# Optimization experiments

Measured on AMD Instinct MI355X. Metric: run time of the kernel, lower is better.

The kernel has to match this reference:

```python
import jax, jax.numpy as jnp
import numpy as np
import math

B, D, OUT = 512, 128, 100000
S, M = 32.0, 0.5
COS_M, SIN_M = math.cos(M), math.sin(M)
TH = math.cos(math.pi - M)
MM = math.sin(math.pi - M) * M
M1 = M2 = M3 = M5 = 1.0


def setup_inputs() -> dict:
    key = jax.random.key(0)
    k1, k2, k3, k4, k5, k6 = jax.random.split(key, 6)
    x = jax.random.normal(k1, (B, D), dtype=jnp.float32)
    label = jax.random.randint(k2, (B,), 0, OUT)
    k = jax.random.uniform(k3, (1, 1, 1024, 1024), dtype=jnp.float32)
    x0 = jax.random.uniform(k4, (1, 3, 112, 96), dtype=jnp.float32)
    img = jax.random.uniform(k5, (1, 3, 112, 96), dtype=jnp.float32)
    # xavier_uniform for [OUT, D]
    limit = math.sqrt(6.0 / (OUT + D))
    W = jax.random.uniform(k6, (OUT, D), minval=-limit, maxval=limit, dtype=jnp.float32)
    return {"x": x, "label": label, "k": k, "x0": x0, "img": img, "W": W}


def _arcmargin(x, W, label):
    xn = x / jnp.linalg.norm(x, axis=-1, keepdims=True)
    wn = W / jnp.linalg.norm(W, axis=-1, keepdims=True)
    cosine = xn @ wn.T                                  # [B, OUT]
    sine = jnp.sqrt(jnp.clip(1.0 - cosine * cosine, 0.0))
    phi = cosine * COS_M - sine * SIN_M
    phi = jnp.where(cosine - TH > 0, phi, cosine - MM)   # easy_margin=False
    one_hot = jax.nn.one_hot(label, OUT, dtype=cosine.dtype)
    logits = S * (one_hot * phi + (1.0 - one_hot) * cosine)
    logp = jax.nn.log_softmax(logits, axis=-1)
    return -jnp.mean(jnp.take_along_axis(logp, label[:, None], axis=1))


def _tv_loss(k):
    h, w = k.shape[-2], k.shape[-1]
    count_h = (h - 1) * w
    count_w = h * (w - 1)
    h_tv = jnp.sum((k[:, :, 1:, :] - k[:, :, :-1, :]) ** 2)
    w_tv = jnp.sum((k[:, :, :, 1:] - k[:, :, :, :-1]) ** 2)
    return -1.0 * 2.0 * (h_tv / count_h + w_tv / count_w)  # weight = -1*loss_weight


def _bin_loss(k):
    # sum over pixels of k^2 + (k-1)^2, / (h*w), then mean over batch/channel
    return jnp.mean(k * k + (k - 1.0) ** 2)


def _inv_loss(k):
    k = jax.lax.stop_gradient(k)  # original detaches before numpy FFT
    mag = jnp.abs(jnp.fft.fftn(k, axes=(-2, -1)))
    return jnp.mean(jnp.sum(mag, axis=(-1, -2)))  # L1 norm over (-1,-2), then mean


def reference(x, label, k, x0, img, W):
    loss = (M1 * _arcmargin(x, W, label)
            + M2 * _tv_loss(k)
            + M3 * _bin_loss(k)
            + M5 * _inv_loss(k))
    return loss
```

## Files before the change

kernel.cpp:

```cpp
#include <hip/hip_runtime.h>


typedef short bf16x8 __attribute__((ext_vector_type(8)));
typedef float f32x4 __attribute__((ext_vector_type(4)));
typedef unsigned short u16;
typedef unsigned int u32;

#define BATCH 512
#define DIM 128
#define OUTN 100000
#define OUTPAD 100096
#define NOBLK 782
#define NROW2 1564
#define CHUNKS 16
#define CHSZ2 98
#define SSCALE 32.0f
#define K2C 46.166241308446828f
#define COSM 0.8775825618903728f
#define SINM 0.479425538604203f
#define THC (-0.8775825618903728f)
#define MMC 0.2397127693021015f

#define S1_FFT 1024
#define S1_TV  2048
#define S1_XP  2176
#define S1_NW  14688

#define S2_GEMM0 256
#define S2_NBLK  3392

__device__ inline u16 f2bf(float f) {
  union { float f; u32 u; } v; v.f = f;
  u32 r = v.u + 0x7FFFu + ((v.u >> 16) & 1u);
  return (u16)(r >> 16);
}

__device__ inline float waveRedSum(float v) {
#pragma unroll
  for (int off = 1; off < 64; off <<= 1) v += __shfl_xor(v, off, 64);
  return v;
}

__device__ inline float halfRedSum(float v) {
#pragma unroll
  for (int off = 1; off < 32; off <<= 1) v += __shfl_xor(v, off, 64);
  return v;
}

__global__ __launch_bounds__(256) void stage1_k(const float* __restrict__ x,
                                                const float* __restrict__ W,
                                                const int* __restrict__ label,
                                                const float* __restrict__ kimg,
                                                u32* __restrict__ xh,
                                                float* __restrict__ coslab,
                                                u32* __restrict__ Wh,
                                                float4* __restrict__ tvpart,
                                                float2* __restrict__ fbuf) {
  __shared__ __align__(16) float smem[2064];
  int t = threadIdx.x;
  int bid = blockIdx.x;

  if (bid < S1_FFT) {
    float* re = smem;
    float* im = smem + 1024;
    int r = bid;
#pragma unroll
    for (int i = 0; i < 4; i++) {
      int idx = i * 256 + t;
      re[idx] = kimg[r * 1024 + idx];
      im[idx] = 0.f;
    }
    __syncthreads();
    for (int lh = 9; lh >= 0; lh--) {
      int hlf = 1 << lh;
      float ang = -6.283185307179586f / (float)(hlf * 2);
#pragma unroll
      for (int i = 0; i < 2; i++) {
        int bf = i * 256 + t;
        int pos = bf & (hlf - 1);
        int g = bf >> lh;
        int i0 = (g << (lh + 1)) + pos;
        int i1 = i0 + hlf;
        float ur = re[i0], ui = im[i0], vr = re[i1], vi = im[i1];
        float s, c;
        __sincosf(ang * (float)pos, &s, &c);
        re[i0] = ur + vr; im[i0] = ui + vi;
        float dr = ur - vr, di = ui - vi;
        re[i1] = dr * c - di * s;
        im[i1] = dr * s + di * c;
      }
      __syncthreads();
    }
#pragma unroll
    for (int i = 0; i < 4; i++) {
      int idx = i * 256 + t;
      fbuf[(size_t)r * 1024 + idx] = make_float2(re[idx], im[idx]);
    }
  } else if (bid < S1_TV) {
    int r = bid - S1_FFT;
    int idx = r * 1024 + t * 4;
    float4 v = *(const float4*)&kimg[idx];
    float bs = v.x * v.x + (v.x - 1.f) * (v.x - 1.f)
             + v.y * v.y + (v.y - 1.f) * (v.y - 1.f)
             + v.z * v.z + (v.z - 1.f) * (v.z - 1.f)
             + v.w * v.w + (v.w - 1.f) * (v.w - 1.f);
    float d0 = v.y - v.x, d1 = v.z - v.y, d2 = v.w - v.z;
    float wsm = d0 * d0 + d1 * d1 + d2 * d2;
    if (t < 255) { float e4 = kimg[idx + 4]; float d3 = e4 - v.w; wsm += d3 * d3; }
    float hs = 0.f;
    if (r < 1023) {
      float4 n = *(const float4*)&kimg[idx + 1024];
      float h0 = n.x - v.x, h1 = n.y - v.y, h2 = n.z - v.z, h3 = n.w - v.w;
      hs = h0 * h0 + h1 * h1 + h2 * h2 + h3 * h3;
    }
    hs = waveRedSum(hs); wsm = waveRedSum(wsm); bs = waveRedSum(bs);
    float (*red)[4] = (float(*)[4])smem;
    if ((t & 63) == 0) { int w = t >> 6; red[0][w] = hs; red[1][w] = wsm; red[2][w] = bs; }
    __syncthreads();
    if (t == 0)
      tvpart[r] = make_float4(red[0][0] + red[0][1] + red[0][2] + red[0][3],
                              red[1][0] + red[1][1] + red[1][2] + red[1][3],
                              red[2][0] + red[2][1] + red[2][2] + red[2][3], 0.f);
  } else if (bid < S1_XP) {
    int b = (bid - S1_TV) * 4 + (t >> 6);
    int lane = t & 63;
    size_t xb = (size_t)b * DIM;
    float2 v = *(const float2*)&x[xb + lane * 2];
    int lab = label[b];
    size_t wb = (size_t)lab * DIM;
    float2 w = *(const float2*)&W[wb + lane * 2];
    float ss = waveRedSum(v.x * v.x + v.y * v.y);
    float d  = waveRedSum(v.x * w.x + v.y * w.y);
    float nw = waveRedSum(w.x * w.x + w.y * w.y);
    float inv = rsqrtf(ss);
    xh[b * 64 + lane] = (u32)f2bf(v.x * inv) | ((u32)f2bf(v.y * inv) << 16);
    if (lane == 0) coslab[b] = d * rsqrtf(ss * nw);
  } else {
    int p = (bid - S1_XP) * 4 + (t >> 6);
    int lane = t & 63;
    if (2 * p >= OUTN) {
      *(uint2*)&Wh[(size_t)p * 128 + lane * 2] = make_uint2(0u, 0u);
      return;
    }
    float4 v = *(const float4*)&W[(size_t)p * 256 + lane * 4];
    float ss = halfRedSum(v.x * v.x + v.y * v.y + v.z * v.z + v.w * v.w);
    float inv = rsqrtf(ss);
    u32 lo = (u32)f2bf(v.x * inv) | ((u32)f2bf(v.y * inv) << 16);
    u32 hi = (u32)f2bf(v.z * inv) | ((u32)f2bf(v.w * inv) << 16);
    *(uint2*)&Wh[(size_t)p * 128 + lane * 2] = make_uint2(lo, hi);
  }
}

__global__ __launch_bounds__(256, 4) void stage2_k(const u16* __restrict__ Wh,
                                                   const u16* __restrict__ xh,
                                                   float* __restrict__ gpart,
                                                   const float2* __restrict__ fbuf,
                                                   float* __restrict__ fftpart) {
  __shared__ __align__(16) char smem[32784];
  int t = threadIdx.x;
  int bid = blockIdx.x;

  if (bid >= S2_GEMM0) {
    int wgrp = (bid - S2_GEMM0) & 31, g = (bid - S2_GEMM0) >> 5;
    int o = g * 8 + (wgrp & 7), bt = wgrp >> 3;
    if (o >= NOBLK) return;
    int o0 = o * 128, b0 = bt * 128;
    u16* Ash = (u16*)smem;
    u16* Bsh = (u16*)(smem + 16384);
    int wv = t >> 6, lane = t & 63;
    int wo = (wv & 1) << 6, wbs = (wv >> 1) << 6;
    int m16 = lane & 15, q = lane >> 4;
    f32x4 acc[4][4] = {};

#pragma unroll
    for (int kc = 0; kc < 2; kc++) {
      if (kc) __syncthreads();
#pragma unroll
      for (int i = 0; i < 4; i++) {
        int f = i * 256 + t;
        int rr = f >> 3, gg = f & 7;
        int sw = ((gg ^ (rr & 7)) * 8);
        *(uint4*)&Ash[rr * 64 + sw] =
            *(const uint4*)&Wh[(size_t)(o0 + rr) * DIM + kc * 64 + gg * 8];
        *(uint4*)&Bsh[rr * 64 + sw] =
            *(const uint4*)&xh[(size_t)(b0 + rr) * DIM + kc * 64 + gg * 8];
      }
      __syncthreads();
#pragma unroll
      for (int kk = 0; kk < 2; kk++) {
        bf16x8 af[4], bfr[4];
#pragma unroll
        for (int i = 0; i < 4; i++) {
          int row = wo + i * 16 + m16;
          af[i] = *(const bf16x8*)&Ash[row * 64 + (((kk * 4 + q) ^ (row & 7)) * 8)];
        }
#pragma unroll
        for (int j = 0; j < 4; j++) {
          int row = wbs + j * 16 + m16;
          bfr[j] = *(const bf16x8*)&Bsh[row * 64 + (((kk * 4 + q) ^ (row & 7)) * 8)];
        }
#pragma unroll
        for (int i = 0; i < 4; i++)
#pragma unroll
          for (int j = 0; j < 4; j++)
            acc[i][j] = __builtin_amdgcn_mfma_f32_16x16x32_bf16(af[i], bfr[j], acc[i][j], 0, 0, 0);
      }
    }
#pragma unroll
    for (int j = 0; j < 4; j++) {
      float s = 0.f;
#pragma unroll
      for (int i = 0; i < 4; i++)
#pragma unroll
        for (int r = 0; r < 4; r++)
          s += exp2f(K2C * acc[i][j][r]);
      s += __shfl_xor(s, 16, 64);
      s += __shfl_xor(s, 32, 64);
      if (q == 0)
        gpart[(size_t)(o * 2 + (wv & 1)) * 512 + b0 + wbs + j * 16 + m16] = s;
    }
  } else {
    float2* arr = (float2*)smem;
    float* red = (float*)(smem + 32768);
    int c0 = bid * 4;
#pragma unroll
    for (int i = 0; i < 16; i++) {
      int li = i * 256 + t;
      int rr = li >> 2, c = li & 3;
      arr[rr * 4 + c] = fbuf[(size_t)rr * 1024 + c0 + c];
    }
    __syncthreads();
    for (int lh = 9; lh >= 0; lh--) {
      int hlf = 1 << lh;
      float ang = -6.283185307179586f / (float)(hlf * 2);
#pragma unroll
      for (int i = 0; i < 8; i++) {
        int w = i * 256 + t;
        int c = w & 3, bf = w >> 2;
        int pos = bf & (hlf - 1), g2i = bf >> lh;
        int i0 = ((g2i << (lh + 1)) + pos) * 4 + c;
        int i1 = i0 + hlf * 4;
        float2 u = arr[i0], v = arr[i1];
        float s, cc;
        __sincosf(ang * (float)pos, &s, &cc);
        arr[i0] = make_float2(u.x + v.x, u.y + v.y);
        float dr = u.x - v.x, di = u.y - v.y;
        arr[i1] = make_float2(dr * cc - di * s, dr * s + di * cc);
      }
      __syncthreads();
    }
    float s = 0.f;
#pragma unroll
    for (int i = 0; i < 16; i++) {
      float2 v = arr[i * 256 + t];
      s += sqrtf(v.x * v.x + v.y * v.y);
    }
    s = waveRedSum(s);
    if ((t & 63) == 0) red[t >> 6] = s;
    __syncthreads();
    if (t == 0) fftpart[bid] = red[0] + red[1] + red[2] + red[3];
  }
}

__global__ __launch_bounds__(256) void gemmred_k(const float* __restrict__ gpart,
                                                 float* __restrict__ g2,
                                                 const u32* __restrict__ xh32,
                                                 const u32* __restrict__ Wh32,
                                                 const int* __restrict__ label,
                                                 float* __restrict__ labexp) {
  int t = threadIdx.x;
  int blk = blockIdx.x;
  if (blk < 32) {
    int chunk = blk >> 1, half = blk & 1;
    int b = half * 256 + t;
    int rBeg = chunk * CHSZ2;
    int rEnd = rBeg + CHSZ2; if (rEnd > NROW2) rEnd = NROW2;
    float s = 0.f;
    for (int r = rBeg; r < rEnd; r++) s += gpart[(size_t)r * 512 + b];
    g2[chunk * 512 + b] = s;
  } else {
    int b = (blk - 32) * 256 + t;
    int lab = label[b];
    const u32* xr = &xh32[b * 64];
    const u32* wr = &Wh32[(size_t)lab * 64];
    float d = 0.f;
#pragma unroll 8
    for (int i = 0; i < 64; i++) {
      u32 xa = xr[i], wa = wr[i];
      float xl = __uint_as_float(xa << 16), xhp = __uint_as_float(xa & 0xFFFF0000u);
      float wl = __uint_as_float(wa << 16), whp = __uint_as_float(wa & 0xFFFF0000u);
      d += xl * wl + xhp * whp;
    }
    labexp[b] = exp2f(K2C * d);
  }
}

__global__ __launch_bounds__(256) void final_k(const float* __restrict__ coslab,
                                               const float* __restrict__ g2,
                                               const float4* __restrict__ tvpart,
                                               const float* __restrict__ fftpart,
                                               const float* __restrict__ labexp,
                                               float* __restrict__ out) {
  int t = threadIdx.x;
  float arc = 0.f, hs = 0.f, wsm = 0.f, bs = 0.f, fs = 0.f;
#pragma unroll
  for (int i = 0; i < 2; i++) {
    int b = i * 256 + t;
    float se = 0.f;
#pragma unroll
    for (int c = 0; c < CHUNKS; c++) se += g2[c * 512 + b];
    se -= 96.0f;
    se -= labexp[b];
    float cl = coslab[b];
    float sine = sqrtf(fmaxf(0.f, 1.f - cl * cl));
    float phi = cl * COSM - sine * SINM;
    if (!(cl - THC > 0.f)) phi = cl - MMC;
    arc += __logf(se + exp2f(K2C * phi)) - SSCALE * phi;
  }
#pragma unroll
  for (int i = 0; i < 4; i++) {
    float4 p = tvpart[i * 256 + t];
    hs += p.x; wsm += p.y; bs += p.z;
  }
  fs = fftpart[t];
  arc = waveRedSum(arc); hs = waveRedSum(hs); wsm = waveRedSum(wsm);
  bs = waveRedSum(bs); fs = waveRedSum(fs);
  __shared__ float red[5][4];
  if ((t & 63) == 0) {
    int w = t >> 6;
    red[0][w] = arc; red[1][w] = hs; red[2][w] = wsm; red[3][w] = bs; red[4][w] = fs;
  }
  __syncthreads();
  if (t == 0) {
    float A = 0, H = 0, Wv = 0, Bv = 0, F = 0;
#pragma unroll
    for (int w = 0; w < 4; w++) {
      A += red[0][w]; H += red[1][w]; Wv += red[2][w]; Bv += red[3][w]; F += red[4][w];
    }
    float cnt = 1023.0f * 1024.0f;
    out[0] = A * (1.0f / 512.0f) - 2.0f * (H / cnt + Wv / cnt)
           + Bv * (1.0f / 1048576.0f) + F;
  }
}

extern "C" void kernel_launch(void* const* d_in, const int* in_sizes, int n_in,
                              void* d_out, int out_size, void* d_ws, size_t ws_size,
                              hipStream_t stream) {
  const float* x = (const float*)d_in[0];
  const int* label = (const int*)d_in[1];
  const float* kimg = (const float*)d_in[2];
  const float* W = (const float*)d_in[5];
  float* out = (float*)d_out;
  char* ws = (char*)d_ws;
  float*  coslab  = (float*)(ws + 0);
  u32*    xh      = (u32*)(ws + 2048);
  u32*    Wh      = (u32*)(ws + 133120);
  float2* fbuf    = (float2*)(ws + 25757696);
  float*  gpart   = (float*)(ws + 34146304);
  float*  g2      = (float*)(ws + 37349376);
  float4* tvpart  = (float4*)(ws + 37382144);
  float*  fftpart = (float*)(ws + 37398528);
  float*  labexp  = (float*)(ws + 37399552);

  hipLaunchKernelGGL(stage1_k, dim3(S1_NW), dim3(256), 0, stream,
                     x, W, label, kimg, xh, coslab, Wh, tvpart, fbuf);
  hipLaunchKernelGGL(stage2_k, dim3(S2_NBLK), dim3(256), 0, stream,
                     (const u16*)Wh, (const u16*)xh, gpart, fbuf, fftpart);
  hipLaunchKernelGGL(gemmred_k, dim3(34), dim3(256), 0, stream,
                     gpart, g2, xh, Wh, label, labexp);
  hipLaunchKernelGGL(final_k, dim3(1), dim3(256), 0, stream,
                     coslab, g2, tvpart, fftpart, labexp, out);
}
```

Measured before the change: 159.7 us.

## Fuse W normalization and bf16 conversion into GEMM tiles, drop Wh buffer

W-row normalization and bf16 packing move out of stage1 and into the GEMM blocks of stage2. Each GEMM block now loads and normalizes its 128 W rows once into a swizzled shared tile, then loops over all four batch tiles. This removes the write and re-read of the 25 MB intermediate Wh buffer and about 12.5k stage1 blocks. The label dot product in gemmred now recomputes the normalized label rows from W. In exchange, shared memory per block grows (occupancy hint 4 to 3) and there are fewer, longer GEMM blocks (782).

```diff
diff --git a/kernel.cpp b/kernel.cpp
--- a/kernel.cpp
+++ b/kernel.cpp
@@ -9,7 +9,6 @@
 #define BATCH 512
 #define DIM 128
 #define OUTN 100000
-#define OUTPAD 100096
 #define NOBLK 782
 #define NROW2 1564
 #define CHUNKS 16
@@ -23,17 +22,18 @@
 
 #define S1_FFT 1024
 #define S1_TV  2048
-#define S1_XP  2176
-#define S1_NW  14688
+#define S1_NB  2176
 
 #define S2_GEMM0 256
-#define S2_NBLK  3392
+#define S2_NBLK  1038
 
 __device__ inline u16 f2bf(float f) {
   union { float f; u32 u; } v; v.f = f;
   u32 r = v.u + 0x7FFFu + ((v.u >> 16) & 1u);
   return (u16)(r >> 16);
 }
+__device__ inline float bflo(u32 u) { return __uint_as_float(u << 16); }
+__device__ inline float bfhi(u32 u) { return __uint_as_float(u & 0xFFFF0000u); }
 
 __device__ inline float waveRedSum(float v) {
 #pragma unroll
@@ -53,7 +53,6 @@
                                                 const float* __restrict__ kimg,
                                                 u32* __restrict__ xh,
                                                 float* __restrict__ coslab,
-                                                u32* __restrict__ Wh,
                                                 float4* __restrict__ tvpart,
                                                 float2* __restrict__ fbuf) {
   __shared__ __align__(16) float smem[2064];
@@ -121,7 +120,7 @@
       tvpart[r] = make_float4(red[0][0] + red[0][1] + red[0][2] + red[0][3],
                               red[1][0] + red[1][1] + red[1][2] + red[1][3],
                               red[2][0] + red[2][1] + red[2][2] + red[2][3], 0.f);
-  } else if (bid < S1_XP) {
+  } else {
     int b = (bid - S1_TV) * 4 + (t >> 6);
     int lane = t & 63;
     size_t xb = (size_t)b * DIM;
@@ -135,93 +134,95 @@
     float inv = rsqrtf(ss);
     xh[b * 64 + lane] = (u32)f2bf(v.x * inv) | ((u32)f2bf(v.y * inv) << 16);
     if (lane == 0) coslab[b] = d * rsqrtf(ss * nw);
-  } else {
-    int p = (bid - S1_XP) * 4 + (t >> 6);
-    int lane = t & 63;
-    if (2 * p >= OUTN) {
-      *(uint2*)&Wh[(size_t)p * 128 + lane * 2] = make_uint2(0u, 0u);
-      return;
-    }
-    float4 v = *(const float4*)&W[(size_t)p * 256 + lane * 4];
-    float ss = halfRedSum(v.x * v.x + v.y * v.y + v.z * v.z + v.w * v.w);
-    float inv = rsqrtf(ss);
-    u32 lo = (u32)f2bf(v.x * inv) | ((u32)f2bf(v.y * inv) << 16);
-    u32 hi = (u32)f2bf(v.z * inv) | ((u32)f2bf(v.w * inv) << 16);
-    *(uint2*)&Wh[(size_t)p * 128 + lane * 2] = make_uint2(lo, hi);
-  }
-}
-
-__global__ __launch_bounds__(256, 4) void stage2_k(const u16* __restrict__ Wh,
-                                                   const u16* __restrict__ xh,
+  }
+}
+
+__global__ __launch_bounds__(256, 3) void stage2_k(const float* __restrict__ W,
+                                                   const u16* __restrict__ xh16,
                                                    float* __restrict__ gpart,
                                                    const float2* __restrict__ fbuf,
                                                    float* __restrict__ fftpart) {
-  __shared__ __align__(16) char smem[32784];
+  __shared__ __align__(16) char smem[49168];
   int t = threadIdx.x;
   int bid = blockIdx.x;
 
   if (bid >= S2_GEMM0) {
-    int wgrp = (bid - S2_GEMM0) & 31, g = (bid - S2_GEMM0) >> 5;
-    int o = g * 8 + (wgrp & 7), bt = wgrp >> 3;
-    if (o >= NOBLK) return;
-    int o0 = o * 128, b0 = bt * 128;
+    int o = bid - S2_GEMM0;
+    int o0 = o * 128;
     u16* Ash = (u16*)smem;
-    u16* Bsh = (u16*)(smem + 16384);
+    u16* Bsh = (u16*)(smem + 32768);
     int wv = t >> 6, lane = t & 63;
     int wo = (wv & 1) << 6, wbs = (wv >> 1) << 6;
     int m16 = lane & 15, q = lane >> 4;
-    f32x4 acc[4][4] = {};
-
-#pragma unroll
-    for (int kc = 0; kc < 2; kc++) {
-      if (kc) __syncthreads();
-#pragma unroll
-      for (int i = 0; i < 4; i++) {
-        int f = i * 256 + t;
-        int rr = f >> 3, gg = f & 7;
-        int sw = ((gg ^ (rr & 7)) * 8);
-        *(uint4*)&Ash[rr * 64 + sw] =
-            *(const uint4*)&Wh[(size_t)(o0 + rr) * DIM + kc * 64 + gg * 8];
-        *(uint4*)&Bsh[rr * 64 + sw] =
-            *(const uint4*)&xh[(size_t)(b0 + rr) * DIM + kc * 64 + gg * 8];
+
+#pragma unroll
+    for (int it = 0; it < 16; it++) {
+      int f = it * 256 + t;
+      int rr = f >> 5, c = f & 31;
+      int grow = o0 + rr;
+      float4 v = make_float4(0.f, 0.f, 0.f, 0.f);
+      if (grow < OUTN) v = *(const float4*)&W[(size_t)grow * DIM + c * 4];
+      float ss = halfRedSum(v.x * v.x + v.y * v.y + v.z * v.z + v.w * v.w);
+      float inv = (grow < OUTN) ? rsqrtf(ss) : 0.f;
+      u32 lo = (u32)f2bf(v.x * inv) | ((u32)f2bf(v.y * inv) << 16);
+      u32 hi = (u32)f2bf(v.z * inv) | ((u32)f2bf(v.w * inv) << 16);
+      int dst = rr * 128 + (((c >> 1) ^ (rr & 15)) << 3) + ((c & 1) << 2);
+      *(uint2*)&Ash[dst] = make_uint2(lo, hi);
+    }
+    __syncthreads();
+
+    for (int bt = 0; bt < 4; bt++) {
+      int b0 = bt * 128;
+      f32x4 acc[4][4] = {};
+#pragma unroll
+      for (int kc = 0; kc < 2; kc++) {
+        if (bt || kc) __syncthreads();
+#pragma unroll
+        for (int i2 = 0; i2 < 4; i2++) {
+          int f = i2 * 256 + t;
+          int rr = f >> 3, gg = f & 7;
+          *(uint4*)&Bsh[rr * 64 + ((gg ^ (rr & 7)) << 3)] =
+              *(const uint4*)&xh16[(size_t)(b0 + rr) * DIM + kc * 64 + gg * 8];
+        }
+        __syncthreads();
+#pragma unroll
+        for (int kkl = 0; kkl < 2; kkl++) {
+          int kk = kc * 2 + kkl;
+          bf16x8 af[4], bfr[4];
+#pragma unroll
+          for (int i = 0; i < 4; i++) {
+            int row = wo + i * 16 + m16;
+            af[i] = *(const bf16x8*)&Ash[row * 128 + ((((kk << 2) + q) ^ (row & 15)) << 3)];
+          }
+#pragma unroll
+          for (int j = 0; j < 4; j++) {
+            int row = wbs + j * 16 + m16;
+            bfr[j] = *(const bf16x8*)&Bsh[row * 64 + ((((kkl << 2) + q) ^ (row & 7)) << 3)];
+          }
+#pragma unroll
+          for (int i = 0; i < 4; i++)
+#pragma unroll
+            for (int j = 0; j < 4; j++)
+              acc[i][j] = __builtin_amdgcn_mfma_f32_16x16x32_bf16(af[i], bfr[j], acc[i][j], 0, 0, 0);
+        }
       }
-      __syncthreads();
-#pragma unroll
-      for (int kk = 0; kk < 2; kk++) {
-        bf16x8 af[4], bfr[4];
-#pragma unroll
-        for (int i = 0; i < 4; i++) {
-          int row = wo + i * 16 + m16;
-          af[i] = *(const bf16x8*)&Ash[row * 64 + (((kk * 4 + q) ^ (row & 7)) * 8)];
-        }
-#pragma unroll
-        for (int j = 0; j < 4; j++) {
-          int row = wbs + j * 16 + m16;
-          bfr[j] = *(const bf16x8*)&Bsh[row * 64 + (((kk * 4 + q) ^ (row & 7)) * 8)];
-        }
+#pragma unroll
+      for (int j = 0; j < 4; j++) {
+        float s = 0.f;
 #pragma unroll
         for (int i = 0; i < 4; i++)
 #pragma unroll
-          for (int j = 0; j < 4; j++)
-            acc[i][j] = __builtin_amdgcn_mfma_f32_16x16x32_bf16(af[i], bfr[j], acc[i][j], 0, 0, 0);
+          for (int r = 0; r < 4; r++)
+            s += exp2f(K2C * acc[i][j][r]);
+        s += __shfl_xor(s, 16, 64);
+        s += __shfl_xor(s, 32, 64);
+        if (q == 0)
+          gpart[(size_t)(o * 2 + (wv & 1)) * 512 + b0 + wbs + j * 16 + m16] = s;
       }
-    }
-#pragma unroll
-    for (int j = 0; j < 4; j++) {
-      float s = 0.f;
-#pragma unroll
-      for (int i = 0; i < 4; i++)
-#pragma unroll
-        for (int r = 0; r < 4; r++)
-          s += exp2f(K2C * acc[i][j][r]);
-      s += __shfl_xor(s, 16, 64);
-      s += __shfl_xor(s, 32, 64);
-      if (q == 0)
-        gpart[(size_t)(o * 2 + (wv & 1)) * 512 + b0 + wbs + j * 16 + m16] = s;
     }
   } else {
     float2* arr = (float2*)smem;
-    float* red = (float*)(smem + 32768);
+    float* red = (float*)(smem + 49152);
     int c0 = bid * 4;
 #pragma unroll
     for (int i = 0; i < 16; i++) {
@@ -265,7 +266,7 @@
 __global__ __launch_bounds__(256) void gemmred_k(const float* __restrict__ gpart,
                                                  float* __restrict__ g2,
                                                  const u32* __restrict__ xh32,
-                                                 const u32* __restrict__ Wh32,
+                                                 const float* __restrict__ W,
                                                  const int* __restrict__ label,
                                                  float* __restrict__ labexp) {
   int t = threadIdx.x;
@@ -279,19 +280,19 @@
     for (int r = rBeg; r < rEnd; r++) s += gpart[(size_t)r * 512 + b];
     g2[chunk * 512 + b] = s;
   } else {
-    int b = (blk - 32) * 256 + t;
+    int b = (blk - 32) * 8 + (t >> 5);
+    int c = t & 31;
     int lab = label[b];
-    const u32* xr = &xh32[b * 64];
-    const u32* wr = &Wh32[(size_t)lab * 64];
-    float d = 0.f;
-#pragma unroll 8
-    for (int i = 0; i < 64; i++) {
-      u32 xa = xr[i], wa = wr[i];
-      float xl = __uint_as_float(xa << 16), xhp = __uint_as_float(xa & 0xFFFF0000u);
-      float wl = __uint_as_float(wa << 16), whp = __uint_as_float(wa & 0xFFFF0000u);
-      d += xl * wl + xhp * whp;
-    }
-    labexp[b] = exp2f(K2C * d);
+    float4 v = *(const float4*)&W[(size_t)lab * DIM + c * 4];
+    float ss = halfRedSum(v.x * v.x + v.y * v.y + v.z * v.z + v.w * v.w);
+    float inv = rsqrtf(ss);
+    u32 lo = (u32)f2bf(v.x * inv) | ((u32)f2bf(v.y * inv) << 16);
+    u32 hi = (u32)f2bf(v.z * inv) | ((u32)f2bf(v.w * inv) << 16);
+    uint2 xv = *(const uint2*)&xh32[b * 32 + c];
+    float d = bflo(xv.x) * bflo(lo) + bfhi(xv.x) * bfhi(lo)
+            + bflo(xv.y) * bflo(hi) + bfhi(xv.y) * bfhi(hi);
+    d = halfRedSum(d);
+    if (c == 0) labexp[b] = exp2f(K2C * d);
   }
 }
 
@@ -354,20 +355,19 @@
   char* ws = (char*)d_ws;
   float*  coslab  = (float*)(ws + 0);
   u32*    xh      = (u32*)(ws + 2048);
-  u32*    Wh      = (u32*)(ws + 133120);
-  float2* fbuf    = (float2*)(ws + 25757696);
-  float*  gpart   = (float*)(ws + 34146304);
-  float*  g2      = (float*)(ws + 37349376);
-  float4* tvpart  = (float4*)(ws + 37382144);
-  float*  fftpart = (float*)(ws + 37398528);
-  float*  labexp  = (float*)(ws + 37399552);
-
-  hipLaunchKernelGGL(stage1_k, dim3(S1_NW), dim3(256), 0, stream,
-                     x, W, label, kimg, xh, coslab, Wh, tvpart, fbuf);
+  float2* fbuf    = (float2*)(ws + 133120);
+  float*  gpart   = (float*)(ws + 8521728);
+  float*  g2      = (float*)(ws + 11724800);
+  float4* tvpart  = (float4*)(ws + 11757568);
+  float*  fftpart = (float*)(ws + 11773952);
+  float*  labexp  = (float*)(ws + 11774976);
+
+  hipLaunchKernelGGL(stage1_k, dim3(S1_NB), dim3(256), 0, stream,
+                     x, W, label, kimg, xh, coslab, tvpart, fbuf);
   hipLaunchKernelGGL(stage2_k, dim3(S2_NBLK), dim3(256), 0, stream,
-                     (const u16*)Wh, (const u16*)xh, gpart, fbuf, fftpart);
-  hipLaunchKernelGGL(gemmred_k, dim3(34), dim3(256), 0, stream,
-                     gpart, g2, xh, Wh, label, labexp);
+                     W, (const u16*)xh, gpart, fbuf, fftpart);
+  hipLaunchKernelGGL(gemmred_k, dim3(96), dim3(256), 0, stream,
+                     gpart, g2, xh, W, label, labexp);
   hipLaunchKernelGGL(final_k, dim3(1), dim3(256), 0, stream,
                      coslab, g2, tvpart, fftpart, labexp, out);
 }
```

Result: slower. 168.8 us (+5.7%).

## Load GEMM fragments directly from global into registers, dropping LDS staging

Applied to the files above, without the earlier changes.

The stage2 GEMM blocks no longer stage W and x tiles through swizzled shared memory with barriers. Each lane now loads its MFMA bf16x8 fragments straight from global memory, double-buffered in registers across four K-steps. Launch bounds drop from 4 to 3 blocks per SM to leave room for the extra registers. This removes LDS traffic and syncs, but each wave now reads its operands from global/L2 with strided row accesses, and tiles shared between waves are fetched redundantly.

```diff
diff --git a/kernel.cpp b/kernel.cpp
--- a/kernel.cpp
+++ b/kernel.cpp
@@ -9,7 +9,6 @@
 #define BATCH 512
 #define DIM 128
 #define OUTN 100000
-#define OUTPAD 100096
 #define NOBLK 782
 #define NROW2 1564
 #define CHUNKS 16
@@ -34,6 +33,8 @@
   u32 r = v.u + 0x7FFFu + ((v.u >> 16) & 1u);
   return (u16)(r >> 16);
 }
+__device__ inline float bflo(u32 u) { return __uint_as_float(u << 16); }
+__device__ inline float bfhi(u32 u) { return __uint_as_float(u & 0xFFFF0000u); }
 
 __device__ inline float waveRedSum(float v) {
 #pragma unroll
@@ -151,8 +152,8 @@
   }
 }
 
-__global__ __launch_bounds__(256, 4) void stage2_k(const u16* __restrict__ Wh,
-                                                   const u16* __restrict__ xh,
+__global__ __launch_bounds__(256, 3) void stage2_k(const u16* __restrict__ Wh,
+                                                   const u16* __restrict__ xh16,
                                                    float* __restrict__ gpart,
                                                    const float2* __restrict__ fbuf,
                                                    float* __restrict__ fftpart) {
@@ -165,46 +166,38 @@
     int o = g * 8 + (wgrp & 7), bt = wgrp >> 3;
     if (o >= NOBLK) return;
     int o0 = o * 128, b0 = bt * 128;
-    u16* Ash = (u16*)smem;
-    u16* Bsh = (u16*)(smem + 16384);
     int wv = t >> 6, lane = t & 63;
     int wo = (wv & 1) << 6, wbs = (wv >> 1) << 6;
     int m16 = lane & 15, q = lane >> 4;
+
+    const u16* Ab = Wh + (size_t)(o0 + wo + m16) * DIM + q * 8;
+    const u16* Bb = xh16 + (size_t)(b0 + wbs + m16) * DIM + q * 8;
+
     f32x4 acc[4][4] = {};
-
-#pragma unroll
-    for (int kc = 0; kc < 2; kc++) {
-      if (kc) __syncthreads();
-#pragma unroll
-      for (int i = 0; i < 4; i++) {
-        int f = i * 256 + t;
-        int rr = f >> 3, gg = f & 7;
-        int sw = ((gg ^ (rr & 7)) * 8);
-        *(uint4*)&Ash[rr * 64 + sw] =
-            *(const uint4*)&Wh[(size_t)(o0 + rr) * DIM + kc * 64 + gg * 8];
-        *(uint4*)&Bsh[rr * 64 + sw] =
-            *(const uint4*)&xh[(size_t)(b0 + rr) * DIM + kc * 64 + gg * 8];
+    bf16x8 aA[4], bA[4], aB[4], bB[4];
+#pragma unroll
+    for (int i = 0; i < 4; i++) {
+      aA[i] = *(const bf16x8*)(Ab + i * 16 * DIM);
+      bA[i] = *(const bf16x8*)(Bb + i * 16 * DIM);
+    }
+#pragma unroll
+    for (int kk = 0; kk < 4; kk++) {
+      bf16x8* ca = (kk & 1) ? aB : aA;
+      bf16x8* cb = (kk & 1) ? bB : bA;
+      bf16x8* na = (kk & 1) ? aA : aB;
+      bf16x8* nb = (kk & 1) ? bA : bB;
+      if (kk < 3) {
+#pragma unroll
+        for (int i = 0; i < 4; i++) {
+          na[i] = *(const bf16x8*)(Ab + (kk + 1) * 32 + i * 16 * DIM);
+          nb[i] = *(const bf16x8*)(Bb + (kk + 1) * 32 + i * 16 * DIM);
+        }
       }
-      __syncthreads();
-#pragma unroll
-      for (int kk = 0; kk < 2; kk++) {
-        bf16x8 af[4], bfr[4];
-#pragma unroll
-        for (int i = 0; i < 4; i++) {
-          int row = wo + i * 16 + m16;
-          af[i] = *(const bf16x8*)&Ash[row * 64 + (((kk * 4 + q) ^ (row & 7)) * 8)];
-        }
-#pragma unroll
-        for (int j = 0; j < 4; j++) {
-          int row = wbs + j * 16 + m16;
-          bfr[j] = *(const bf16x8*)&Bsh[row * 64 + (((kk * 4 + q) ^ (row & 7)) * 8)];
-        }
-#pragma unroll
-        for (int i = 0; i < 4; i++)
-#pragma unroll
-          for (int j = 0; j < 4; j++)
-            acc[i][j] = __builtin_amdgcn_mfma_f32_16x16x32_bf16(af[i], bfr[j], acc[i][j], 0, 0, 0);
-      }
+#pragma unroll
+      for (int i = 0; i < 4; i++)
+#pragma unroll
+        for (int j = 0; j < 4; j++)
+          acc[i][j] = __builtin_amdgcn_mfma_f32_16x16x32_bf16(ca[i], cb[j], acc[i][j], 0, 0, 0);
     }
 #pragma unroll
     for (int j = 0; j < 4; j++) {
@@ -287,9 +280,7 @@
 #pragma unroll 8
     for (int i = 0; i < 64; i++) {
       u32 xa = xr[i], wa = wr[i];
-      float xl = __uint_as_float(xa << 16), xhp = __uint_as_float(xa & 0xFFFF0000u);
-      float wl = __uint_as_float(wa << 16), whp = __uint_as_float(wa & 0xFFFF0000u);
-      d += xl * wl + xhp * whp;
+      d += bflo(xa) * bflo(wa) + bfhi(xa) * bfhi(wa);
     }
     labexp[b] = exp2f(K2C * d);
   }
```

Result: slower. 185.4 us (+16.1%).
